# Optimization experiments

Hardware: AMD Instinct MI355X
Metric: run time of the kernel (lower is better)

The kernel has to match this reference:

```python
import jax, jax.numpy as jnp
import numpy as np

NS, NV = 128, 64        # multiplicities of 0e and 1o node irreps
TPC = NS + NV           # 192: tp-out channels for each of 0e and 1o
N_NODES, N_EDGES, NUM_BASIS = 16000, 256000, 16
INV_SQRT3 = 1.0 / np.sqrt(3.0).astype(np.float32)


def setup_inputs() -> dict:
    key = jax.random.key(0)
    ks = jax.random.split(key, 12)
    return {
        "node_feat": jax.random.normal(ks[0], (N_NODES, NS + 3 * NV), jnp.float32),
        "edge_attr": jax.random.normal(ks[1], (N_EDGES, NUM_BASIS), jnp.float32),
        "edge_rshs": jax.random.normal(ks[2], (N_EDGES, 4), jnp.float32),
        "edge_index": jax.random.randint(ks[3], (2, N_EDGES), 0, N_NODES, jnp.int64 if jax.config.jax_enable_x64 else jnp.int32),
        "W_pre_s": jax.random.normal(ks[4], (NS, NS), jnp.float32),
        "b_pre_s": jnp.zeros((NS,), jnp.float32),
        "W_pre_v": jax.random.normal(ks[5], (NV, NV), jnp.float32),
        "W1": jax.random.normal(ks[6], (NUM_BASIS, 128), jnp.float32),
        "b1": jnp.zeros((128,), jnp.float32),
        "W2": jax.random.normal(ks[7], (128, 2 * (NS + NV)), jnp.float32),
        "b2": jnp.zeros((2 * (NS + NV),), jnp.float32),
        "W_post_s": jax.random.normal(ks[8], (TPC, NS), jnp.float32),
        "W_post_v": jax.random.normal(ks[9], (TPC, NV), jnp.float32),
    }


def reference(node_feat, edge_attr, edge_rshs, edge_index,
              W_pre_s, b_pre_s, W_pre_v, W1, b1, W2, b2, W_post_s, W_post_v):
    n = node_feat.shape[0]
    s = node_feat[:, :NS]                       # [N,128] scalars (0e)
    v = node_feat[:, NS:].reshape(n, NV, 3)     # [N,64,3] vectors (1o)

    # lin_node_pre (irrep-wise linear, bias on scalars only, fan-in normalized)
    x_s = s @ W_pre_s * (1.0 / np.sqrt(NS)) + b_pre_s
    x_v = jnp.einsum("nuc,uv->nvc", v, W_pre_v) * (1.0 / np.sqrt(NV))

    dst, src = edge_index[0], edge_index[1]
    s_j = x_s[src]                              # gather [E,128]
    v_j = x_v[src]                              # gather [E,64,3]
    r0 = edge_rshs[:, :1]                       # [E,1]  0e sph-harm
    r1 = edge_rshs[:, 1:4]                      # [E,3]  1o sph-harm

    # per-edge TP weights from radial MLP: 16 -> 128 -> silu -> 384
    h = jax.nn.silu(edge_attr @ W1 + b1)
    w = h @ W2 + b2                             # [E,384]
    w_ss0 = w[:, :NS]                           # (0e x 0e -> 0e), 128
    w_vv0 = w[:, NS:NS + NV]                    # (1o x 1o -> 0e), 64
    w_sv1 = w[:, NS + NV:2 * NS + NV]           # (0e x 1o -> 1o), 128
    w_vs1 = w[:, 2 * NS + NV:]                  # (1o x 0e -> 1o), 64

    # uvu tensor product (CG: 1 for l=0 couplings, 1/sqrt(3) for 1x1->0)
    msg_s = jnp.concatenate([
        w_ss0 * s_j * r0,                                        # [E,128]
        w_vv0 * jnp.einsum("euc,ec->eu", v_j, r1) * INV_SQRT3,   # [E,64]
    ], axis=-1)                                                  # [E,192]
    msg_v = jnp.concatenate([
        (w_sv1 * s_j)[:, :, None] * r1[:, None, :],              # [E,128,3]
        w_vs1[:, :, None] * v_j * r0[:, :, None],                # [E,64,3]
    ], axis=1)                                                   # [E,192,3]

    # scatter-reduce messages to destination nodes
    acc_s = jax.ops.segment_sum(msg_s, dst, num_segments=n)      # [N,192]
    acc_v = jax.ops.segment_sum(msg_v, dst, num_segments=n)      # [N,192,3]

    # gate activation: silu on scalars, norm-sigmoid gating on vectors
    g_s = jax.nn.silu(acc_s)
    v_norm = jnp.sqrt(jnp.sum(acc_v * acc_v, axis=-1) + 1e-12)   # [N,192]
    g_v = acc_v * jax.nn.sigmoid(v_norm)[:, :, None]

    # lin_node_post back to node irreps
    p_s = g_s @ W_post_s * (1.0 / np.sqrt(TPC))
    p_v = jnp.einsum("nuc,uv->nvc", g_v, W_post_v) * (1.0 / np.sqrt(TPC))

    out_s = x_s + p_s
    out_v = x_v + p_v
    return jnp.concatenate([out_s, out_v.reshape(n, NV * 3)], axis=-1)
```

## Files before the change

kernel.cpp:

```cpp
#include <hip/hip_runtime.h>
#include <hip/hip_bf16.h>

#define NS 128
#define NV 64
#define TPC 192
#define NBASIS 16
#define HID 128
#define WOUT 384
#define NNODE 16000
#define NEDGE 256000
#define EPB 32
#define GVPLANE 3072000
#define VPLANE  1024000

typedef __attribute__((ext_vector_type(8))) short bf16x8;
typedef __attribute__((ext_vector_type(8))) unsigned short u16x8;
typedef __attribute__((ext_vector_type(4))) unsigned short u16x4;
typedef __attribute__((ext_vector_type(4))) float f32x4;

__device__ __forceinline__ float silu_f(float x) { return x / (1.0f + __expf(-x)); }
__device__ __forceinline__ unsigned short bf16b(float x) {
  __hip_bfloat16 h = __float2bfloat16(x);
  return *reinterpret_cast<unsigned short*>(&h);
}
__device__ __forceinline__ float bf2f(unsigned short u) {
  return __uint_as_float(((unsigned)u) << 16);
}

__global__ __launch_bounds__(256) void pack_weights(
    const float* __restrict__ W1, const float* __restrict__ W2,
    const float* __restrict__ Wqs, const float* __restrict__ Wqv,
    unsigned short* __restrict__ W1P, unsigned short* __restrict__ W2P,
    unsigned short* __restrict__ WqsP, unsigned short* __restrict__ WqvP,
    int* __restrict__ cursor) {
  const int id = blockIdx.x * 256 + threadIdx.x;
  const int j = id & 7, lane = (id >> 3) & 63;
  const int kj = (lane >> 4) * 8 + j;
  const int nc = lane & 15;
  if (id < NNODE) cursor[id] = 0;
  if (id < 24 * 4 * 64 * 8) {
    const int kc = (id >> 9) & 3, nt = id >> 11;
    W2P[id] = bf16b(W2[(kc * 32 + kj) * WOUT + nt * 16 + nc]);
  }
  if (id < 8 * 64 * 8) {
    const int nt = id >> 9;
    W1P[id] = (kj < NBASIS) ? bf16b(W1[kj * HID + nt * 16 + nc]) : (unsigned short)0;
  }
  if (id < 8 * 6 * 64 * 8) {
    const int kc = (id >> 9) % 6, nt = id / (6 * 512);
    WqsP[id] = bf16b(Wqs[(kc * 32 + kj) * NS + nt * 16 + nc]);
  }
  if (id < 4 * 6 * 64 * 8) {
    const int kc = (id >> 9) % 6, nt = id / (6 * 512);
    WqvP[id] = bf16b(Wqv[(kc * 32 + kj) * NV + nt * 16 + nc]);
  }
}

__global__ __launch_bounds__(256) void node_pre4(
    const float* __restrict__ node_feat, const float* __restrict__ Wps,
    const float* __restrict__ bps, const float* __restrict__ Wpv,
    float* __restrict__ x_s, float* __restrict__ x_v,
    unsigned short* __restrict__ x_s16, unsigned short* __restrict__ xv16) {
  const int n0 = blockIdx.x * 4;
  const int t = threadIdx.x;
  __shared__ float s_sh[4][NS];
  __shared__ float v_sh[4][NV * 3];
  for (int i = t; i < 4 * 320; i += 256) {
    const int nn = i / 320, off = i - nn * 320;
    const float val = node_feat[(size_t)(n0 + nn) * 320 + off];
    if (off < NS) s_sh[nn][off] = val; else v_sh[nn][off - NS] = val;
  }
  __syncthreads();
  for (int o = t; o < 320; o += 256) {
    if (o < NS) {
      float a0 = 0.f, a1 = 0.f, a2 = 0.f, a3 = 0.f;
      #pragma unroll 8
      for (int u = 0; u < NS; ++u) {
        const float wv = Wps[u * NS + o];
        a0 = fmaf(s_sh[0][u], wv, a0); a1 = fmaf(s_sh[1][u], wv, a1);
        a2 = fmaf(s_sh[2][u], wv, a2); a3 = fmaf(s_sh[3][u], wv, a3);
      }
      const float b = bps[o];
      const float r0 = a0 * 0.08838834764831845f + b;
      const float r1 = a1 * 0.08838834764831845f + b;
      const float r2 = a2 * 0.08838834764831845f + b;
      const float r3 = a3 * 0.08838834764831845f + b;
      x_s[(size_t)(n0 + 0) * NS + o] = r0; x_s16[(size_t)(n0 + 0) * NS + o] = bf16b(r0);
      x_s[(size_t)(n0 + 1) * NS + o] = r1; x_s16[(size_t)(n0 + 1) * NS + o] = bf16b(r1);
      x_s[(size_t)(n0 + 2) * NS + o] = r2; x_s16[(size_t)(n0 + 2) * NS + o] = bf16b(r2);
      x_s[(size_t)(n0 + 3) * NS + o] = r3; x_s16[(size_t)(n0 + 3) * NS + o] = bf16b(r3);
    } else {
      const int q = o - NS;
      const int vch = q / 3, c = q - vch * 3;
      float a0 = 0.f, a1 = 0.f, a2 = 0.f, a3 = 0.f;
      #pragma unroll 8
      for (int u = 0; u < NV; ++u) {
        const float wv = Wpv[u * NV + vch];
        a0 = fmaf(v_sh[0][u * 3 + c], wv, a0); a1 = fmaf(v_sh[1][u * 3 + c], wv, a1);
        a2 = fmaf(v_sh[2][u * 3 + c], wv, a2); a3 = fmaf(v_sh[3][u * 3 + c], wv, a3);
      }
      const float r0 = a0 * 0.125f, r1 = a1 * 0.125f, r2 = a2 * 0.125f, r3 = a3 * 0.125f;
      x_v[(size_t)(n0 + 0) * (NV * 3) + q] = r0;
      x_v[(size_t)(n0 + 1) * (NV * 3) + q] = r1;
      x_v[(size_t)(n0 + 2) * (NV * 3) + q] = r2;
      x_v[(size_t)(n0 + 3) * (NV * 3) + q] = r3;
      unsigned short* pl = xv16 + (size_t)c * VPLANE;
      pl[(size_t)(n0 + 0) * NV + vch] = bf16b(r0);
      pl[(size_t)(n0 + 1) * NV + vch] = bf16b(r1);
      pl[(size_t)(n0 + 2) * NV + vch] = bf16b(r2);
      pl[(size_t)(n0 + 3) * NV + vch] = bf16b(r3);
    }
  }
}

__global__ void hist_kernel(const int* __restrict__ ei, int* __restrict__ cnt) {
  int e = blockIdx.x * 256 + threadIdx.x;
  if (e < NEDGE) atomicAdd(&cnt[ei[e]], 1);
}

__global__ __launch_bounds__(256) void scan_kernel(
    const int* __restrict__ cnt, int* __restrict__ row_start, int* __restrict__ cursor) {
  __shared__ int part[256];
  const int t = threadIdx.x;
  const int base = t * 63;
  int s = 0;
  for (int i = 0; i < 63; ++i) {
    int idx = base + i;
    if (idx < NNODE) s += cnt[idx];
  }
  part[t] = s;
  __syncthreads();
  if (t == 0) {
    int run = 0;
    for (int i = 0; i < 256; ++i) { int x = part[i]; part[i] = run; run += x; }
  }
  __syncthreads();
  int run = part[t];
  for (int i = 0; i < 63; ++i) {
    int idx = base + i;
    if (idx < NNODE) {
      int c = cnt[idx];
      row_start[idx] = run;
      cursor[idx] = run;
      run += c;
    }
  }
  if (t == 255) row_start[NNODE] = run;
}

__global__ void scatter_kernel(const int* __restrict__ ei,
                               const float* __restrict__ edge_rshs,
                               int* __restrict__ cursor, int* __restrict__ perm,
                               float4* __restrict__ meta) {
  int e = blockIdx.x * 256 + threadIdx.x;
  if (e < NEDGE) {
    int p = atomicAdd(&cursor[ei[e]], 1);
    perm[e] = p;
    float4 m;
    m.x = __int_as_float(ei[NEDGE + e]);
    m.y = edge_rshs[e * 4 + 1];
    m.z = edge_rshs[e * 4 + 2];
    m.w = edge_rshs[e * 4 + 3];
    meta[p] = m;
  }
}

__global__ __launch_bounds__(256) void edge_mlp_mfma(
    const float* __restrict__ edge_attr, const float* __restrict__ edge_rshs,
    const int* __restrict__ edge_index, const int* __restrict__ perm,
    const unsigned short* __restrict__ W1P, const float* __restrict__ b1,
    const unsigned short* __restrict__ W2P, const float* __restrict__ b2,
    const unsigned short* __restrict__ x_s16, const unsigned short* __restrict__ xv16,
    unsigned short* __restrict__ msg) {
  union SMU {
    struct { unsigned short ea[32 * 48]; unsigned short Hs[32 * 136]; } p1;
    unsigned short msgb[32 * 392];
  };
  __shared__ __align__(16) SMU sm;
  __shared__ __align__(16) unsigned short sj[32][136];
  __shared__ __align__(16) unsigned short vd[32][72];
  __shared__ unsigned short b2s[384];
  __shared__ unsigned short b1s[128];
  __shared__ int src_sh[32];
  __shared__ int slot_sh[32];
  __shared__ float rsh_sh[32][4];
  const int t = threadIdx.x;
  const int lane = t & 63;
  const int w = t >> 6;
  const int l15 = lane & 15;
  const int l4 = lane >> 4;
  const int eblk = blockIdx.x * EPB;

  if (t < 32 * 4) rsh_sh[t >> 2][t & 3] = edge_rshs[(size_t)eblk * 4 + t];
  if (t < 32) {
    src_sh[t] = edge_index[NEDGE + eblk + t];
    slot_sh[t] = perm[eblk + t];
  }
  for (int i = t; i < 384; i += 256) b2s[i] = bf16b(b2[i]);
  if (t < 128) b1s[t] = bf16b(b1[t]);
  if (t < 128) {
    const int e = t >> 2, q = t & 3;
    const float4 v = *(const float4*)&edge_attr[(size_t)(eblk + e) * NBASIS + q * 4];
    u16x4 tmp;
    tmp[0] = bf16b(v.x); tmp[1] = bf16b(v.y); tmp[2] = bf16b(v.z); tmp[3] = bf16b(v.w);
    *(u16x4*)&sm.p1.ea[e * 48 + q * 4] = tmp;
  } else {
    const int idx = t - 128;
    const int e = idx >> 2, q = idx & 3;
    *(u16x8*)&sm.p1.ea[e * 48 + 16 + q * 8] = (u16x8){0, 0, 0, 0, 0, 0, 0, 0};
  }
  __syncthreads();

  {
    const int mt = w & 1, ch = w >> 1;
    const bf16x8 afrag = *(const bf16x8*)&sm.p1.ea[(mt * 16 + l15) * 48 + l4 * 8];
    #pragma unroll
    for (int nt = 0; nt < 4; ++nt) {
      const int ntg = ch * 4 + nt;
      const bf16x8 bfrag = *(const bf16x8*)&W1P[((size_t)ntg * 64 + lane) * 8];
      const int col = ntg * 16 + l15;
      const float bias = bf2f(b1s[col]);
      f32x4 d = {bias, bias, bias, bias};
      d = __builtin_amdgcn_mfma_f32_16x16x32_bf16(afrag, bfrag, d, 0, 0, 0);
      #pragma unroll
      for (int i = 0; i < 4; ++i) {
        const int e = mt * 16 + l4 * 4 + i;
        sm.p1.Hs[e * 136 + col] = bf16b(silu_f(d[i]));
      }
    }
  }
  #pragma unroll
  for (int p = 0; p < 2; ++p) {
    const int idx = p * 256 + t;
    const int e = idx >> 4, c8 = idx & 15;
    *(u16x8*)&sj[e][c8 * 8] =
        *(const u16x8*)&x_s16[(size_t)src_sh[e] * NS + c8 * 8];
  }
  #pragma unroll
  for (int p = 0; p < 8; ++p) {
    const int idx = p * 256 + t;
    const int e = idx >> 6, u = idx & 63;
    const size_t base = (size_t)src_sh[e] * NV + u;
    const float v0 = bf2f(xv16[base]);
    const float v1 = bf2f(xv16[VPLANE + base]);
    const float v2 = bf2f(xv16[2 * VPLANE + base]);
    const float dotv = fmaf(v0, rsh_sh[e][1], fmaf(v1, rsh_sh[e][2], v2 * rsh_sh[e][3]));
    vd[e][u] = bf16b(dotv * 0.5773502691896258f);
  }
  __syncthreads();

  bf16x8 afr[2][4];
  #pragma unroll
  for (int mt = 0; mt < 2; ++mt)
    #pragma unroll
    for (int k = 0; k < 4; ++k)
      afr[mt][k] = *(const bf16x8*)&sm.p1.Hs[(mt * 16 + l15) * 136 + k * 32 + l4 * 8];

  float r0a[2][4];
  #pragma unroll
  for (int mt = 0; mt < 2; ++mt)
    #pragma unroll
    for (int i = 0; i < 4; ++i) r0a[mt][i] = rsh_sh[mt * 16 + l4 * 4 + i][0];
  __syncthreads();

  #pragma unroll
  for (int nn = 0; nn < 6; ++nn) {
    const int nt = w * 6 + nn;
    bf16x8 bfr[4];
    #pragma unroll
    for (int k = 0; k < 4; ++k)
      bfr[k] = *(const bf16x8*)&W2P[(((size_t)nt * 4 + k) * 64 + lane) * 8];
    const int col = nt * 16 + l15;
    const float bias = bf2f(b2s[col]);
    f32x4 acc0 = {bias, bias, bias, bias}, acc1 = {bias, bias, bias, bias};
    #pragma unroll
    for (int k = 0; k < 4; ++k) {
      acc0 = __builtin_amdgcn_mfma_f32_16x16x32_bf16(afr[0][k], bfr[k], acc0, 0, 0, 0);
      acc1 = __builtin_amdgcn_mfma_f32_16x16x32_bf16(afr[1][k], bfr[k], acc1, 0, 0, 0);
    }
    if (col < NS) {
      #pragma unroll
      for (int mt = 0; mt < 2; ++mt)
        #pragma unroll
        for (int i = 0; i < 4; ++i) {
          const int e = mt * 16 + l4 * 4 + i;
          const float wv = mt ? acc1[i] : acc0[i];
          sm.msgb[e * 392 + col] = bf16b(wv * bf2f(sj[e][col]) * r0a[mt][i]);
        }
    } else if (col < NS + NV) {
      const int u = col - NS;
      #pragma unroll
      for (int mt = 0; mt < 2; ++mt)
        #pragma unroll
        for (int i = 0; i < 4; ++i) {
          const int e = mt * 16 + l4 * 4 + i;
          const float wv = mt ? acc1[i] : acc0[i];
          sm.msgb[e * 392 + col] = bf16b(wv * bf2f(vd[e][u]));
        }
    } else if (col < 2 * NS + NV) {
      const int sjc = col - (NS + NV);
      #pragma unroll
      for (int mt = 0; mt < 2; ++mt)
        #pragma unroll
        for (int i = 0; i < 4; ++i) {
          const int e = mt * 16 + l4 * 4 + i;
          const float wv = mt ? acc1[i] : acc0[i];
          sm.msgb[e * 392 + col] = bf16b(wv * bf2f(sj[e][sjc]));
        }
    } else {
      #pragma unroll
      for (int mt = 0; mt < 2; ++mt)
        #pragma unroll
        for (int i = 0; i < 4; ++i) {
          const int e = mt * 16 + l4 * 4 + i;
          const float wv = mt ? acc1[i] : acc0[i];
          sm.msgb[e * 392 + col] = bf16b(wv * r0a[mt][i]);
        }
    }
  }
  __syncthreads();

  #pragma unroll
  for (int p = 0; p < 6; ++p) {
    const int idx = p * 256 + t;
    const int e = idx / 48, c = idx - e * 48;
    const u16x8 vv = *(const u16x8*)&sm.msgb[e * 392 + c * 8];
    *(u16x8*)&msg[(size_t)slot_sh[e] * 384 + c * 8] = vv;
  }
}

__global__ __launch_bounds__(256) void node_gather(
    const unsigned short* __restrict__ msg, const int* __restrict__ row_start,
    const float4* __restrict__ meta, const unsigned short* __restrict__ xv16,
    unsigned short* __restrict__ gs16, unsigned short* __restrict__ gv16) {
  const int n = blockIdx.x;
  const int t = threadIdx.x;
  const int role = t >> 6, ln = t & 63;
  const int beg = row_start[n], end = row_start[n + 1];

  float a0 = 0.f, a1 = 0.f, a2 = 0.f;

  if (role == 0) {
    const unsigned short* mp = msg + (size_t)beg * 384;
    int i = beg;
    for (; i + 8 <= end; i += 8, mp += 3072) {
      unsigned int pr[8]; unsigned short v2[8];
      #pragma unroll
      for (int u = 0; u < 8; ++u) {
        pr[u] = *(const unsigned int*)(mp + u * 384 + 2 * ln);
        v2[u] = mp[u * 384 + 128 + ln];
      }
      #pragma unroll
      for (int u = 0; u < 8; ++u) {
        a0 += __uint_as_float(pr[u] << 16);
        a1 += __uint_as_float(pr[u] & 0xffff0000u);
        a2 += bf2f(v2[u]);
      }
    }
    for (; i < end; ++i, mp += 384) {
      const unsigned int p = *(const unsigned int*)(mp + 2 * ln);
      a0 += __uint_as_float(p << 16);
      a1 += __uint_as_float(p & 0xffff0000u);
      a2 += bf2f(mp[128 + ln]);
    }
    gs16[(size_t)n * 192 + 2 * ln]     = bf16b(silu_f(a0));
    gs16[(size_t)n * 192 + 2 * ln + 1] = bf16b(silu_f(a1));
    gs16[(size_t)n * 192 + 128 + ln]   = bf16b(silu_f(a2));
  } else {
    if (role < 3) {
      const unsigned short* mp = msg + (size_t)beg * 384 + 192 + (role - 1) * 64 + ln;
      int i = beg;
      for (; i + 8 <= end; i += 8, mp += 3072) {
        float4 mt[8]; unsigned short v[8];
        #pragma unroll
        for (int u = 0; u < 8; ++u) { mt[u] = meta[i + u]; v[u] = mp[u * 384]; }
        #pragma unroll
        for (int u = 0; u < 8; ++u) {
          const float m = bf2f(v[u]);
          a0 = fmaf(m, mt[u].y, a0);
          a1 = fmaf(m, mt[u].z, a1);
          a2 = fmaf(m, mt[u].w, a2);
        }
      }
      for (; i < end; ++i, mp += 384) {
        const float4 mt = meta[i];
        const float m = bf2f(mp[0]);
        a0 = fmaf(m, mt.y, a0); a1 = fmaf(m, mt.z, a1); a2 = fmaf(m, mt.w, a2);
      }
    } else {
      const unsigned short* mp = msg + (size_t)beg * 384 + 320 + ln;
      int i = beg;
      for (; i + 8 <= end; i += 8, mp += 3072) {
        float4 mt[8]; unsigned short v[8];
        #pragma unroll
        for (int u = 0; u < 8; ++u) { mt[u] = meta[i + u]; v[u] = mp[u * 384]; }
        unsigned short x0[8], x1[8], x2[8];
        #pragma unroll
        for (int u = 0; u < 8; ++u) {
          const size_t base = (size_t)__float_as_int(mt[u].x) * NV + ln;
          x0[u] = xv16[base]; x1[u] = xv16[VPLANE + base]; x2[u] = xv16[2 * VPLANE + base];
        }
        #pragma unroll
        for (int u = 0; u < 8; ++u) {
          const float m = bf2f(v[u]);
          a0 = fmaf(m, bf2f(x0[u]), a0);
          a1 = fmaf(m, bf2f(x1[u]), a1);
          a2 = fmaf(m, bf2f(x2[u]), a2);
        }
      }
      for (; i < end; ++i, mp += 384) {
        const float4 mt = meta[i];
        const float m = bf2f(mp[0]);
        const size_t base = (size_t)__float_as_int(mt.x) * NV + ln;
        a0 = fmaf(m, bf2f(xv16[base]), a0);
        a1 = fmaf(m, bf2f(xv16[VPLANE + base]), a1);
        a2 = fmaf(m, bf2f(xv16[2 * VPLANE + base]), a2);
      }
    }
    const float nrm = sqrtf(fmaf(a0, a0, fmaf(a1, a1, a2 * a2)) + 1e-12f);
    const float sg = 1.f / (1.f + __expf(-nrm));
    const int u = (role < 3) ? (role - 1) * 64 + ln : 128 + ln;
    gv16[(size_t)0 * GVPLANE + (size_t)n * 192 + u] = bf16b(a0 * sg);
    gv16[(size_t)1 * GVPLANE + (size_t)n * 192 + u] = bf16b(a1 * sg);
    gv16[(size_t)2 * GVPLANE + (size_t)n * 192 + u] = bf16b(a2 * sg);
  }
}

__global__ __launch_bounds__(256) void node_post_mfma(
    const unsigned short* __restrict__ gs16, const unsigned short* __restrict__ gv16,
    const unsigned short* __restrict__ WqsP, const unsigned short* __restrict__ WqvP,
    const float* __restrict__ x_s, const float* __restrict__ x_v,
    float* __restrict__ out) {
  __shared__ __align__(16) unsigned short gsA[32 * 200];
  __shared__ __align__(16) unsigned short gvA[3][32 * 200];
  const int n0 = blockIdx.x * 32;
  const int t = threadIdx.x;
  const int lane = t & 63;
  const int w = t >> 6;
  const int l15 = lane & 15;
  const int l4 = lane >> 4;
  const float SC = 0.07216878364870323f;

  {
    const unsigned short* sp = gs16 + (size_t)n0 * 192;
    for (int idx = t; idx < 768; idx += 256) {
      const int row = idx / 24, ch = idx - row * 24;
      *(u16x8*)&gsA[row * 200 + ch * 8] = *(const u16x8*)&sp[row * 192 + ch * 8];
    }
    #pragma unroll
    for (int c = 0; c < 3; ++c) {
      const unsigned short* vp = gv16 + (size_t)c * GVPLANE + (size_t)n0 * 192;
      for (int idx = t; idx < 768; idx += 256) {
        const int row = idx / 24, ch = idx - row * 24;
        *(u16x8*)&gvA[c][row * 200 + ch * 8] = *(const u16x8*)&vp[row * 192 + ch * 8];
      }
    }
  }
  __syncthreads();

  f32x4 accS[2][2];
  f32x4 accV[3][2];
  #pragma unroll
  for (int j = 0; j < 2; ++j)
    #pragma unroll
    for (int mt = 0; mt < 2; ++mt) accS[j][mt] = (f32x4){0.f, 0.f, 0.f, 0.f};
  #pragma unroll
  for (int c = 0; c < 3; ++c)
    #pragma unroll
    for (int mt = 0; mt < 2; ++mt) accV[c][mt] = (f32x4){0.f, 0.f, 0.f, 0.f};

  #pragma unroll
  for (int kc = 0; kc < 6; ++kc) {
    bf16x8 aS[2], aV[3][2];
    #pragma unroll
    for (int mt = 0; mt < 2; ++mt)
      aS[mt] = *(const bf16x8*)&gsA[(mt * 16 + l15) * 200 + kc * 32 + l4 * 8];
    #pragma unroll
    for (int c = 0; c < 3; ++c)
      #pragma unroll
      for (int mt = 0; mt < 2; ++mt)
        aV[c][mt] = *(const bf16x8*)&gvA[c][(mt * 16 + l15) * 200 + kc * 32 + l4 * 8];
    const bf16x8 bS0 = *(const bf16x8*)&WqsP[(((size_t)(w * 2 + 0) * 6 + kc) * 64 + lane) * 8];
    const bf16x8 bS1 = *(const bf16x8*)&WqsP[(((size_t)(w * 2 + 1) * 6 + kc) * 64 + lane) * 8];
    const bf16x8 bV  = *(const bf16x8*)&WqvP[(((size_t)w * 6 + kc) * 64 + lane) * 8];
    #pragma unroll
    for (int mt = 0; mt < 2; ++mt) {
      accS[0][mt] = __builtin_amdgcn_mfma_f32_16x16x32_bf16(aS[mt], bS0, accS[0][mt], 0, 0, 0);
      accS[1][mt] = __builtin_amdgcn_mfma_f32_16x16x32_bf16(aS[mt], bS1, accS[1][mt], 0, 0, 0);
    }
    #pragma unroll
    for (int c = 0; c < 3; ++c)
      #pragma unroll
      for (int mt = 0; mt < 2; ++mt)
        accV[c][mt] = __builtin_amdgcn_mfma_f32_16x16x32_bf16(aV[c][mt], bV, accV[c][mt], 0, 0, 0);
  }

  #pragma unroll
  for (int j = 0; j < 2; ++j) {
    const int col = (w * 2 + j) * 16 + l15;
    #pragma unroll
    for (int mt = 0; mt < 2; ++mt)
      #pragma unroll
      for (int i = 0; i < 4; ++i) {
        const int row = n0 + mt * 16 + l4 * 4 + i;
        out[(size_t)row * 320 + col] =
            x_s[(size_t)row * NS + col] + accS[j][mt][i] * SC;
      }
  }
  {
    const int vch = w * 16 + l15;
    #pragma unroll
    for (int mt = 0; mt < 2; ++mt)
      #pragma unroll
      for (int i = 0; i < 4; ++i) {
        const int row = n0 + mt * 16 + l4 * 4 + i;
        const float* xvp = x_v + (size_t)row * (NV * 3) + vch * 3;
        float o0 = xvp[0] + accV[0][mt][i] * SC;
        float o1 = xvp[1] + accV[1][mt][i] * SC;
        float o2 = xvp[2] + accV[2][mt][i] * SC;
        float* op = out + (size_t)row * 320 + NS + vch * 3;
        op[0] = o0; op[1] = o1; op[2] = o2;
      }
  }
}

extern "C" void kernel_launch(void* const* d_in, const int* in_sizes, int n_in,
                              void* d_out, int out_size, void* d_ws, size_t ws_size,
                              hipStream_t stream) {
  const float* node_feat = (const float*)d_in[0];
  const float* edge_attr = (const float*)d_in[1];
  const float* edge_rshs = (const float*)d_in[2];
  const int*   edge_index = (const int*)d_in[3];
  const float* Wps = (const float*)d_in[4];
  const float* bps = (const float*)d_in[5];
  const float* Wpv = (const float*)d_in[6];
  const float* W1  = (const float*)d_in[7];
  const float* b1  = (const float*)d_in[8];
  const float* W2  = (const float*)d_in[9];
  const float* b2  = (const float*)d_in[10];
  const float* Wqs = (const float*)d_in[11];
  const float* Wqv = (const float*)d_in[12];
  float* out = (float*)d_out;

  float* x_s = (float*)d_ws;
  float* x_v = x_s + (size_t)NNODE * NS;
  unsigned short* msg = (unsigned short*)(x_v + (size_t)NNODE * NV * 3);
  unsigned short* W1P = msg + (size_t)NEDGE * 384;
  unsigned short* W2P = W1P + 8 * 64 * 8;
  unsigned short* WqsP = W2P + 24 * 4 * 64 * 8;
  unsigned short* WqvP = WqsP + 8 * 6 * 64 * 8;
  unsigned short* x_s16 = WqvP + 4 * 6 * 64 * 8;
  unsigned short* xv16 = x_s16 + (size_t)NNODE * NS;
  unsigned short* gs16 = xv16 + (size_t)3 * VPLANE;
  unsigned short* gv16 = gs16 + (size_t)NNODE * 192;
  float4* meta = (float4*)(gv16 + (size_t)3 * GVPLANE);
  int* row_start = (int*)(meta + NEDGE);
  int* cursor = row_start + (NNODE + 1);
  int* perm = cursor + NNODE;

  pack_weights<<<192, 256, 0, stream>>>(W1, W2, Wqs, Wqv, W1P, W2P, WqsP, WqvP,
      cursor);
  node_pre4<<<NNODE / 4, 256, 0, stream>>>(node_feat, Wps, bps, Wpv, x_s, x_v,
      x_s16, xv16);
  hist_kernel<<<(NEDGE + 255) / 256, 256, 0, stream>>>(edge_index, cursor);
  scan_kernel<<<1, 256, 0, stream>>>(cursor, row_start, cursor);
  scatter_kernel<<<(NEDGE + 255) / 256, 256, 0, stream>>>(edge_index, edge_rshs,
      cursor, perm, meta);
  edge_mlp_mfma<<<NEDGE / EPB, 256, 0, stream>>>(edge_attr, edge_rshs, edge_index,
      perm, W1P, b1, W2P, b2, x_s16, xv16, msg);
  node_gather<<<NNODE, 256, 0, stream>>>(msg, row_start, meta, xv16, gs16, gv16);
  node_post_mfma<<<NNODE / 32, 256, 0, stream>>>(gs16, gv16, WqsP, WqvP,
      x_s, x_v, out);
}
```

Before: 276.4 us.

## Replace scalar node pre-linear with bf16 MFMA kernel and fold scales into weights

The FP32 scalar-FMA node_pre4 kernel, which handled 4 nodes per block, is replaced by node_pre_mfma. The new kernel handles 32 nodes per block and uses bf16 16x16x32 MFMA with weights pre-packed and pre-scaled in pack_weights. The post-linear normalization constant is also folded into the packed Wqs/Wqv weights, which removes a multiply in node_post_mfma. Node features and the pre-linear weights now go through bf16, so the fp32 x_s/x_v residual path loses precision.

```diff
diff --git a/kernel.cpp b/kernel.cpp
--- a/kernel.cpp
+++ b/kernel.cpp
@@ -30,13 +30,16 @@
 __global__ __launch_bounds__(256) void pack_weights(
     const float* __restrict__ W1, const float* __restrict__ W2,
     const float* __restrict__ Wqs, const float* __restrict__ Wqv,
+    const float* __restrict__ Wps, const float* __restrict__ Wpv,
     unsigned short* __restrict__ W1P, unsigned short* __restrict__ W2P,
     unsigned short* __restrict__ WqsP, unsigned short* __restrict__ WqvP,
+    unsigned short* __restrict__ WpsP, unsigned short* __restrict__ WpvP,
     int* __restrict__ cursor) {
   const int id = blockIdx.x * 256 + threadIdx.x;
   const int j = id & 7, lane = (id >> 3) & 63;
   const int kj = (lane >> 4) * 8 + j;
   const int nc = lane & 15;
+  const float SC = 0.07216878364870323f;
   if (id < NNODE) cursor[id] = 0;
   if (id < 24 * 4 * 64 * 8) {
     const int kc = (id >> 9) & 3, nt = id >> 11;
@@ -48,68 +51,125 @@
   }
   if (id < 8 * 6 * 64 * 8) {
     const int kc = (id >> 9) % 6, nt = id / (6 * 512);
-    WqsP[id] = bf16b(Wqs[(kc * 32 + kj) * NS + nt * 16 + nc]);
+    WqsP[id] = bf16b(Wqs[(kc * 32 + kj) * NS + nt * 16 + nc] * SC);
   }
   if (id < 4 * 6 * 64 * 8) {
     const int kc = (id >> 9) % 6, nt = id / (6 * 512);
-    WqvP[id] = bf16b(Wqv[(kc * 32 + kj) * NV + nt * 16 + nc]);
-  }
-}
-
-__global__ __launch_bounds__(256) void node_pre4(
-    const float* __restrict__ node_feat, const float* __restrict__ Wps,
-    const float* __restrict__ bps, const float* __restrict__ Wpv,
+    WqvP[id] = bf16b(Wqv[(kc * 32 + kj) * NV + nt * 16 + nc] * SC);
+  }
+  if (id < 8 * 4 * 64 * 8) {
+    const int kc = (id >> 9) & 3, nt = id >> 11;
+    WpsP[id] = bf16b(Wps[(kc * 32 + kj) * NS + nt * 16 + nc] * 0.08838834764831845f);
+  }
+  if (id < 4 * 2 * 64 * 8) {
+    const int kc = (id >> 9) & 1, nt = id >> 10;
+    WpvP[id] = bf16b(Wpv[(kc * 32 + kj) * NV + nt * 16 + nc] * 0.125f);
+  }
+}
+
+__global__ __launch_bounds__(256) void node_pre_mfma(
+    const float* __restrict__ node_feat, const float* __restrict__ bps,
+    const unsigned short* __restrict__ WpsP, const unsigned short* __restrict__ WpvP,
     float* __restrict__ x_s, float* __restrict__ x_v,
     unsigned short* __restrict__ x_s16, unsigned short* __restrict__ xv16) {
-  const int n0 = blockIdx.x * 4;
+  __shared__ __align__(16) unsigned short as_[32 * 136];
+  __shared__ __align__(16) unsigned short avp[3][32 * 72];
+  const int n0 = blockIdx.x * 32;
   const int t = threadIdx.x;
-  __shared__ float s_sh[4][NS];
-  __shared__ float v_sh[4][NV * 3];
-  for (int i = t; i < 4 * 320; i += 256) {
-    const int nn = i / 320, off = i - nn * 320;
-    const float val = node_feat[(size_t)(n0 + nn) * 320 + off];
-    if (off < NS) s_sh[nn][off] = val; else v_sh[nn][off - NS] = val;
-  }
-  __syncthreads();
-  for (int o = t; o < 320; o += 256) {
-    if (o < NS) {
-      float a0 = 0.f, a1 = 0.f, a2 = 0.f, a3 = 0.f;
-      #pragma unroll 8
-      for (int u = 0; u < NS; ++u) {
-        const float wv = Wps[u * NS + o];
-        a0 = fmaf(s_sh[0][u], wv, a0); a1 = fmaf(s_sh[1][u], wv, a1);
-        a2 = fmaf(s_sh[2][u], wv, a2); a3 = fmaf(s_sh[3][u], wv, a3);
-      }
-      const float b = bps[o];
-      const float r0 = a0 * 0.08838834764831845f + b;
-      const float r1 = a1 * 0.08838834764831845f + b;
-      const float r2 = a2 * 0.08838834764831845f + b;
-      const float r3 = a3 * 0.08838834764831845f + b;
-      x_s[(size_t)(n0 + 0) * NS + o] = r0; x_s16[(size_t)(n0 + 0) * NS + o] = bf16b(r0);
-      x_s[(size_t)(n0 + 1) * NS + o] = r1; x_s16[(size_t)(n0 + 1) * NS + o] = bf16b(r1);
-      x_s[(size_t)(n0 + 2) * NS + o] = r2; x_s16[(size_t)(n0 + 2) * NS + o] = bf16b(r2);
-      x_s[(size_t)(n0 + 3) * NS + o] = r3; x_s16[(size_t)(n0 + 3) * NS + o] = bf16b(r3);
-    } else {
-      const int q = o - NS;
-      const int vch = q / 3, c = q - vch * 3;
-      float a0 = 0.f, a1 = 0.f, a2 = 0.f, a3 = 0.f;
-      #pragma unroll 8
-      for (int u = 0; u < NV; ++u) {
-        const float wv = Wpv[u * NV + vch];
-        a0 = fmaf(v_sh[0][u * 3 + c], wv, a0); a1 = fmaf(v_sh[1][u * 3 + c], wv, a1);
-        a2 = fmaf(v_sh[2][u * 3 + c], wv, a2); a3 = fmaf(v_sh[3][u * 3 + c], wv, a3);
-      }
-      const float r0 = a0 * 0.125f, r1 = a1 * 0.125f, r2 = a2 * 0.125f, r3 = a3 * 0.125f;
-      x_v[(size_t)(n0 + 0) * (NV * 3) + q] = r0;
-      x_v[(size_t)(n0 + 1) * (NV * 3) + q] = r1;
-      x_v[(size_t)(n0 + 2) * (NV * 3) + q] = r2;
-      x_v[(size_t)(n0 + 3) * (NV * 3) + q] = r3;
-      unsigned short* pl = xv16 + (size_t)c * VPLANE;
-      pl[(size_t)(n0 + 0) * NV + vch] = bf16b(r0);
-      pl[(size_t)(n0 + 1) * NV + vch] = bf16b(r1);
-      pl[(size_t)(n0 + 2) * NV + vch] = bf16b(r2);
-      pl[(size_t)(n0 + 3) * NV + vch] = bf16b(r3);
-    }
+  const int lane = t & 63;
+  const int w = t >> 6;
+  const int l15 = lane & 15;
+  const int l4 = lane >> 4;
+
+  #pragma unroll
+  for (int p = 0; p < 4; ++p) {
+    const int idx = p * 256 + t;
+    const int r = idx >> 5, c4 = idx & 31;
+    const float4 v = *(const float4*)&node_feat[(size_t)(n0 + r) * 320 + c4 * 4];
+    u16x4 tmp;
+    tmp[0] = bf16b(v.x); tmp[1] = bf16b(v.y); tmp[2] = bf16b(v.z); tmp[3] = bf16b(v.w);
+    *(u16x4*)&as_[r * 136 + c4 * 4] = tmp;
+  }
+  #pragma unroll
+  for (int p = 0; p < 8; ++p) {
+    const int idx = p * 256 + t;
+    const int r = idx >> 6, u = idx & 63;
+    const float* vp = &node_feat[(size_t)(n0 + r) * 320 + 128 + u * 3];
+    avp[0][r * 72 + u] = bf16b(vp[0]);
+    avp[1][r * 72 + u] = bf16b(vp[1]);
+    avp[2][r * 72 + u] = bf16b(vp[2]);
+  }
+  __syncthreads();
+
+  f32x4 accS[2][2];
+  #pragma unroll
+  for (int jj = 0; jj < 2; ++jj) {
+    const float b = bps[(w * 2 + jj) * 16 + l15];
+    #pragma unroll
+    for (int mt = 0; mt < 2; ++mt) accS[jj][mt] = (f32x4){b, b, b, b};
+  }
+  f32x4 accV[3][2];
+  #pragma unroll
+  for (int c = 0; c < 3; ++c)
+    #pragma unroll
+    for (int mt = 0; mt < 2; ++mt) accV[c][mt] = (f32x4){0.f, 0.f, 0.f, 0.f};
+
+  #pragma unroll
+  for (int kc = 0; kc < 4; ++kc) {
+    bf16x8 aS[2];
+    #pragma unroll
+    for (int mt = 0; mt < 2; ++mt)
+      aS[mt] = *(const bf16x8*)&as_[(mt * 16 + l15) * 136 + kc * 32 + l4 * 8];
+    const bf16x8 bS0 = *(const bf16x8*)&WpsP[(((size_t)(w * 2 + 0) * 4 + kc) * 64 + lane) * 8];
+    const bf16x8 bS1 = *(const bf16x8*)&WpsP[(((size_t)(w * 2 + 1) * 4 + kc) * 64 + lane) * 8];
+    #pragma unroll
+    for (int mt = 0; mt < 2; ++mt) {
+      accS[0][mt] = __builtin_amdgcn_mfma_f32_16x16x32_bf16(aS[mt], bS0, accS[0][mt], 0, 0, 0);
+      accS[1][mt] = __builtin_amdgcn_mfma_f32_16x16x32_bf16(aS[mt], bS1, accS[1][mt], 0, 0, 0);
+    }
+  }
+  #pragma unroll
+  for (int kc = 0; kc < 2; ++kc) {
+    const bf16x8 bV = *(const bf16x8*)&WpvP[(((size_t)w * 2 + kc) * 64 + lane) * 8];
+    #pragma unroll
+    for (int c = 0; c < 3; ++c) {
+      bf16x8 aV[2];
+      #pragma unroll
+      for (int mt = 0; mt < 2; ++mt)
+        aV[mt] = *(const bf16x8*)&avp[c][(mt * 16 + l15) * 72 + kc * 32 + l4 * 8];
+      #pragma unroll
+      for (int mt = 0; mt < 2; ++mt)
+        accV[c][mt] = __builtin_amdgcn_mfma_f32_16x16x32_bf16(aV[mt], bV, accV[c][mt], 0, 0, 0);
+    }
+  }
+
+  #pragma unroll
+  for (int jj = 0; jj < 2; ++jj) {
+    const int col = (w * 2 + jj) * 16 + l15;
+    #pragma unroll
+    for (int mt = 0; mt < 2; ++mt)
+      #pragma unroll
+      for (int i = 0; i < 4; ++i) {
+        const int row = n0 + mt * 16 + l4 * 4 + i;
+        const float r = accS[jj][mt][i];
+        x_s[(size_t)row * NS + col] = r;
+        x_s16[(size_t)row * NS + col] = bf16b(r);
+      }
+  }
+  {
+    const int vch = w * 16 + l15;
+    #pragma unroll
+    for (int mt = 0; mt < 2; ++mt)
+      #pragma unroll
+      for (int i = 0; i < 4; ++i) {
+        const int row = n0 + mt * 16 + l4 * 4 + i;
+        const float r0 = accV[0][mt][i], r1 = accV[1][mt][i], r2 = accV[2][mt][i];
+        float* xp = x_v + (size_t)row * (NV * 3) + vch * 3;
+        xp[0] = r0; xp[1] = r1; xp[2] = r2;
+        xv16[(size_t)0 * VPLANE + (size_t)row * NV + vch] = bf16b(r0);
+        xv16[(size_t)1 * VPLANE + (size_t)row * NV + vch] = bf16b(r1);
+        xv16[(size_t)2 * VPLANE + (size_t)row * NV + vch] = bf16b(r2);
+      }
   }
 }
 
@@ -439,7 +499,6 @@
   const int w = t >> 6;
   const int l15 = lane & 15;
   const int l4 = lane >> 4;
-  const float SC = 0.07216878364870323f;
 
   {
     const unsigned short* sp = gs16 + (size_t)n0 * 192;
@@ -504,7 +563,7 @@
       for (int i = 0; i < 4; ++i) {
         const int row = n0 + mt * 16 + l4 * 4 + i;
         out[(size_t)row * 320 + col] =
-            x_s[(size_t)row * NS + col] + accS[j][mt][i] * SC;
+            x_s[(size_t)row * NS + col] + accS[j][mt][i];
       }
   }
   {
@@ -515,9 +574,9 @@
       for (int i = 0; i < 4; ++i) {
         const int row = n0 + mt * 16 + l4 * 4 + i;
         const float* xvp = x_v + (size_t)row * (NV * 3) + vch * 3;
-        float o0 = xvp[0] + accV[0][mt][i] * SC;
-        float o1 = xvp[1] + accV[1][mt][i] * SC;
-        float o2 = xvp[2] + accV[2][mt][i] * SC;
+        float o0 = xvp[0] + accV[0][mt][i];
+        float o1 = xvp[1] + accV[1][mt][i];
+        float o2 = xvp[2] + accV[2][mt][i];
         float* op = out + (size_t)row * 320 + NS + vch * 3;
         op[0] = o0; op[1] = o1; op[2] = o2;
       }
@@ -549,7 +608,9 @@
   unsigned short* W2P = W1P + 8 * 64 * 8;
   unsigned short* WqsP = W2P + 24 * 4 * 64 * 8;
   unsigned short* WqvP = WqsP + 8 * 6 * 64 * 8;
-  unsigned short* x_s16 = WqvP + 4 * 6 * 64 * 8;
+  unsigned short* WpsP = WqvP + 4 * 6 * 64 * 8;
+  unsigned short* WpvP = WpsP + 8 * 4 * 64 * 8;
+  unsigned short* x_s16 = WpvP + 4 * 2 * 64 * 8;
   unsigned short* xv16 = x_s16 + (size_t)NNODE * NS;
   unsigned short* gs16 = xv16 + (size_t)3 * VPLANE;
   unsigned short* gv16 = gs16 + (size_t)NNODE * 192;
@@ -558,10 +619,10 @@
   int* cursor = row_start + (NNODE + 1);
   int* perm = cursor + NNODE;
 
-  pack_weights<<<192, 256, 0, stream>>>(W1, W2, Wqs, Wqv, W1P, W2P, WqsP, WqvP,
-      cursor);
-  node_pre4<<<NNODE / 4, 256, 0, stream>>>(node_feat, Wps, bps, Wpv, x_s, x_v,
-      x_s16, xv16);
+  pack_weights<<<192, 256, 0, stream>>>(W1, W2, Wqs, Wqv, Wps, Wpv,
+      W1P, W2P, WqsP, WqvP, WpsP, WpvP, cursor);
+  node_pre_mfma<<<NNODE / 32, 256, 0, stream>>>(node_feat, bps, WpsP, WpvP,
+      x_s, x_v, x_s16, xv16);
   hist_kernel<<<(NEDGE + 255) / 256, 256, 0, stream>>>(edge_index, cursor);
   scan_kernel<<<1, 256, 0, stream>>>(cursor, row_start, cursor);
   scatter_kernel<<<(NEDGE + 255) / 256, 256, 0, stream>>>(edge_index, edge_rshs,
```

Result: faster. 252.1 us (-8.8%).
